# Kernel optimization log

Hardware: AMD Instinct MI355X
Metric: run time of the kernel (lower is better)

## Reference

```python
import jax, jax.numpy as jnp
import numpy as np

N_HEAD = 16
EPS = 1e-6


def setup_inputs() -> dict:
    key = jax.random.key(0)
    k1, k2, k3 = jax.random.split(key, 3)
    B, T, C = 2, 2048, 1024
    x = jax.random.normal(k1, (B, T, C), dtype=jnp.float32)
    w_attn = jax.random.normal(k2, (C, 3 * C), dtype=jnp.float32) * 0.02
    w_proj = jax.random.normal(k3, (C, C), dtype=jnp.float32) * 0.02
    return {"x": x, "w_attn": w_attn, "w_proj": w_proj}


def _linear_attention(q, k, v):
    """q,k,v: (T,B,H,D) with q,k already feature-mapped (elu+1).
    Causal linear attention via a D x D running-state recurrence (same math
    as cumsum of k-v outer products, computed without the O(T*D^2) tensor)."""
    B, H, D = q.shape[1], q.shape[2], q.shape[3]

    def step(carry, qkv_t):
        S, z = carry                      # S:(B,H,D,D), z:(B,H,D)
        qt, kt, vt = qkv_t                # each (B,H,D)
        S = S + kt[..., :, None] * vt[..., None, :]
        z = z + kt
        num = jnp.einsum('bhi,bhij->bhj', qt, S)
        den = jnp.sum(qt * z, axis=-1, keepdims=True)
        return (S, z), num / (den + EPS)

    S0 = jnp.zeros((B, H, D, D), q.dtype)
    z0 = jnp.zeros((B, H, D), q.dtype)
    _, y = jax.lax.scan(step, (S0, z0), (q, k, v))
    return y                              # (T,B,H,D)


def reference(x, w_attn, w_proj):
    B, T, C = x.shape
    H = N_HEAD
    D = C // H
    qkv = x @ w_attn                      # (B,T,3C)
    q, k, v = jnp.split(qkv, 3, axis=-1)

    def to_tbhd(a):                       # (B,T,C) -> (T,B,H,D)
        return a.reshape(B, T, H, D).transpose(1, 0, 2, 3)

    q = jax.nn.elu(to_tbhd(q)) + 1.0      # phi(x) = ELU(x)+1
    k = jax.nn.elu(to_tbhd(k)) + 1.0
    v = to_tbhd(v)

    y = _linear_attention(q, k, v)        # (T,B,H,D)
    y = y.transpose(1, 0, 2, 3).reshape(B, T, C)
    return y @ w_proj                     # resid dropout p=0.0 is identity
```

## Files before the change

kernel.cpp:

```cpp
#include <hip/hip_runtime.h>
#include <hip/hip_bf16.h>
#include <cmath>

#define TB   2048
#define CCH  1024
#define NCH  32
#define EPSF 1e-6f

typedef unsigned short u16;
typedef __attribute__((ext_vector_type(8))) short  frag8;
typedef __attribute__((ext_vector_type(4))) float  floatx4;

__device__ __forceinline__ u16 f2bf(float f) {
    unsigned int u = __float_as_uint(f);
    unsigned int r = (u + 0x7fffu + ((u >> 16) & 1u)) >> 16;
    return (u16)r;
}
__device__ __forceinline__ float bf2f(u16 v) {
    return __uint_as_float(((unsigned int)v) << 16);
}

__device__ __forceinline__ void async_load16(const u16* g, u16* l) {
    __builtin_amdgcn_global_load_lds(
        (const __attribute__((address_space(1))) void*)g,
        (__attribute__((address_space(3))) void*)l,
        16, 0, 0);
}

__global__ __launch_bounds__(256) void prep_k(
    const float* __restrict__ x, const float* __restrict__ wa,
    const float* __restrict__ wp,
    u16* __restrict__ xb, u16* __restrict__ waT, u16* __restrict__ wpT)
{
    __shared__ u16 t[64][72];
    int blk = blockIdx.x;
    if (blk < 2048) {
        int i = (blk * 256 + threadIdx.x) * 8;
        float4 a = *(const float4*)(x + i);
        float4 b = *(const float4*)(x + i + 4);
        u16 v[8];
        v[0] = f2bf(a.x); v[1] = f2bf(a.y); v[2] = f2bf(a.z); v[3] = f2bf(a.w);
        v[4] = f2bf(b.x); v[5] = f2bf(b.y); v[6] = f2bf(b.z); v[7] = f2bf(b.w);
        *(uint4*)(xb + i) = *(uint4*)v;
        return;
    }
    const float* in; u16* out; int K, N, bx, by;
    if (blk < 2048 + 768) {
        int tb = blk - 2048; in = wa; out = waT; K = 1024; N = 3072;
        bx = tb % 48; by = tb / 48;
    } else {
        int tb = blk - 2816; in = wp; out = wpT; K = 1024; N = 1024;
        bx = tb & 15; by = tb >> 4;
    }
    const int k0 = by * 64, n0 = bx * 64;
    #pragma unroll
    for (int i = 0; i < 4; ++i) {
        int rr = (threadIdx.x >> 4) + 16 * i;
        int c4 = (threadIdx.x & 15) * 4;
        float4 v = *(const float4*)(in + (size_t)(k0 + rr) * N + n0 + c4);
        t[c4 + 0][rr] = f2bf(v.x);
        t[c4 + 1][rr] = f2bf(v.y);
        t[c4 + 2][rr] = f2bf(v.z);
        t[c4 + 3][rr] = f2bf(v.w);
    }
    __syncthreads();
    #pragma unroll
    for (int i = 0; i < 2; ++i) {
        int rr = (threadIdx.x >> 3) + 32 * i;
        int c8 = (threadIdx.x & 7) * 8;
        u16 o[8];
        #pragma unroll
        for (int q = 0; q < 8; ++q) o[q] = t[rr][c8 + q];
        *(uint4*)(out + (size_t)(n0 + rr) * K + k0 + c8) = *(uint4*)o;
    }
}

__global__ __launch_bounds__(256) void gemm_bf16_bf16out_k(
    const u16* __restrict__ A, const u16* __restrict__ BT,
    u16* __restrict__ C, int N, int K, int phi_cols)
{
    __shared__ u16 Als[2][128 * 64];
    __shared__ u16 Bls[2][128 * 64];
    const int tid  = threadIdx.x;
    const int wave = tid >> 6, lane = tid & 63;
    const int quad = lane >> 4, lrow = lane & 15;
    const int wm = wave >> 1, wn = wave & 1;
    const int row0 = blockIdx.y * 128, col0 = blockIdx.x * 128;
    const int lr = lane >> 3;
    const int lc = ((lane & 7) ^ lr) * 8;
    const int rsw = lrow & 7;
    floatx4 acc[4][4] = {};
    const int NT = K >> 6;

    #pragma unroll
    for (int m = 0; m < 4; ++m) {
        int i = wave * 4 + m;
        async_load16(A  + (size_t)(row0 + i * 8 + lr) * K + lc, &Als[0][i * 512]);
        async_load16(BT + (size_t)(col0 + i * 8 + lr) * K + lc, &Bls[0][i * 512]);
    }

    for (int t = 0; t < NT; ++t) {
        const int p = t & 1;
        if (t + 1 < NT) {
            const int k0 = (t + 1) << 6;
            #pragma unroll
            for (int m = 0; m < 4; ++m) {
                int i = wave * 4 + m;
                async_load16(A  + (size_t)(row0 + i * 8 + lr) * K + k0 + lc,
                             &Als[p ^ 1][i * 512]);
                async_load16(BT + (size_t)(col0 + i * 8 + lr) * K + k0 + lc,
                             &Bls[p ^ 1][i * 512]);
            }
            __builtin_amdgcn_sched_barrier(0);
            asm volatile("s_waitcnt vmcnt(8)" ::: "memory");
        } else {
            asm volatile("s_waitcnt vmcnt(0)" ::: "memory");
        }
        __builtin_amdgcn_s_barrier();
        __builtin_amdgcn_sched_barrier(0);

        #pragma unroll
        for (int ksi = 0; ksi < 2; ++ksi) {
            frag8 af[4], bf[4];
            #pragma unroll
            for (int i = 0; i < 4; ++i)
                af[i] = *(const frag8*)&Als[p][(wm * 64 + i * 16 + lrow) * 64
                                              + ((ksi * 4 + quad) ^ rsw) * 8];
            #pragma unroll
            for (int i = 0; i < 4; ++i)
                bf[i] = *(const frag8*)&Bls[p][(wn * 64 + i * 16 + lrow) * 64
                                              + ((ksi * 4 + quad) ^ rsw) * 8];
            #pragma unroll
            for (int i = 0; i < 4; ++i)
                #pragma unroll
                for (int jn = 0; jn < 4; ++jn)
                    acc[i][jn] = __builtin_amdgcn_mfma_f32_16x16x32_bf16(
                        af[i], bf[jn], acc[i][jn], 0, 0, 0);
        }

        asm volatile("s_waitcnt lgkmcnt(0)" ::: "memory");
        __builtin_amdgcn_sched_barrier(0);
        __builtin_amdgcn_s_barrier();
    }

    #pragma unroll
    for (int i = 0; i < 4; ++i) {
        #pragma unroll
        for (int jn = 0; jn < 4; ++jn) {
            int col = col0 + wn * 64 + jn * 16 + lrow;
            bool isphi = col < phi_cols;
            #pragma unroll
            for (int r = 0; r < 4; ++r) {
                int row = row0 + wm * 64 + i * 16 + quad * 4 + r;
                float v = acc[i][jn][r];
                if (isphi) v = (v > 0.f) ? (v + 1.f) : __expf(v);
                C[(size_t)row * N + col] = f2bf(v);
            }
        }
    }
}

__global__ __launch_bounds__(256) void gemm_bf16_f32out_k(
    const u16* __restrict__ A, const u16* __restrict__ BT,
    float* __restrict__ C, int N, int K)
{
    __shared__ u16 Als[128 * 128];
    __shared__ u16 Bls[64 * 128];
    const int tid  = threadIdx.x;
    const int wave = tid >> 6, lane = tid & 63;
    const int quad = lane >> 4, lrow = lane & 15;
    const int wm = wave >> 1, wn = wave & 1;
    const int row0 = blockIdx.y * 128, col0 = blockIdx.x * 64;
    const int lr4 = lane >> 4;
    floatx4 acc[4][2] = {};

    for (int k0 = 0; k0 < K; k0 += 128) {
        __syncthreads();
        #pragma unroll
        for (int m = 0; m < 8; ++m) {
            int rbase = wave * 32 + m * 4;
            int cg = (lane & 15) ^ ((rbase + lr4) & 15);
            async_load16(A + (size_t)(row0 + rbase + lr4) * K + k0 + cg * 8,
                         &Als[rbase * 128]);
        }
        #pragma unroll
        for (int m = 0; m < 4; ++m) {
            int rbase = wave * 16 + m * 4;
            int cg = (lane & 15) ^ ((rbase + lr4) & 15);
            async_load16(BT + (size_t)(col0 + rbase + lr4) * K + k0 + cg * 8,
                         &Bls[rbase * 128]);
        }
        __syncthreads();
        #pragma unroll
        for (int ksi = 0; ksi < 4; ++ksi) {
            frag8 af[4], bf[2];
            #pragma unroll
            for (int i = 0; i < 4; ++i)
                af[i] = *(const frag8*)&Als[(wm * 64 + i * 16 + lrow) * 128
                                            + ((ksi * 4 + quad) ^ lrow) * 8];
            #pragma unroll
            for (int jn = 0; jn < 2; ++jn)
                bf[jn] = *(const frag8*)&Bls[(wn * 32 + jn * 16 + lrow) * 128
                                             + ((ksi * 4 + quad) ^ lrow) * 8];
            #pragma unroll
            for (int i = 0; i < 4; ++i)
                #pragma unroll
                for (int jn = 0; jn < 2; ++jn)
                    acc[i][jn] = __builtin_amdgcn_mfma_f32_16x16x32_bf16(
                        af[i], bf[jn], acc[i][jn], 0, 0, 0);
        }
    }

    #pragma unroll
    for (int i = 0; i < 4; ++i)
        #pragma unroll
        for (int jn = 0; jn < 2; ++jn) {
            int col = col0 + wn * 32 + jn * 16 + lrow;
            #pragma unroll
            for (int r = 0; r < 4; ++r) {
                int row = row0 + wm * 64 + i * 16 + quad * 4 + r;
                C[(size_t)row * N + col] = acc[i][jn][r];
            }
        }
}

__global__ __launch_bounds__(256) void chunk_kv_mfma_k(
    const u16* __restrict__ qkv,
    u16* __restrict__ Spt,
    float* __restrict__ zloc,
    u16* __restrict__ VtG)
{
    __shared__ u16 Kt[64][72];
    __shared__ u16 Vt[64][72];
    const int tid  = threadIdx.x;
    const int wave = tid >> 6, lane = tid & 63;
    const int quad = lane >> 4, lrow = lane & 15;
    const int blk = blockIdx.x;
    const int c = blk & 31, h = (blk >> 5) & 15, b = blk >> 9;
    const int t0 = c * 64;
    const u16* base = qkv + (size_t)(b * TB + t0) * 3072 + h * 64;

    #pragma unroll
    for (int m = 0; m < 2; ++m) {
        int chunk = tid + 256 * m;
        int s = chunk >> 3, d0 = (chunk & 7) * 8;
        const u16* row = base + (size_t)s * 3072;
        u16 kv[8], vv[8];
        *(uint4*)kv = *(const uint4*)(row + 1024 + d0);
        *(uint4*)vv = *(const uint4*)(row + 2048 + d0);
        #pragma unroll
        for (int q = 0; q < 8; ++q) { Kt[d0 + q][s] = kv[q]; Vt[d0 + q][s] = vv[q]; }
    }
    __syncthreads();

    #pragma unroll
    for (int m = 0; m < 2; ++m) {
        int e = tid + 256 * m;
        int r = e >> 3, c8 = (e & 7) * 8;
        u16 o[8];
        #pragma unroll
        for (int q = 0; q < 8; ++q) o[q] = Vt[r][c8 + q];
        *(uint4*)(VtG + (size_t)blk * 4096 + r * 64 + c8) = *(uint4*)o;
    }

    frag8 vf[2];
    #pragma unroll
    for (int ks = 0; ks < 2; ++ks)
        vf[ks] = *(const frag8*)&Vt[wave * 16 + lrow][ks * 32 + quad * 8];
    u16* So = Spt + (size_t)blk * 4096;
    #pragma unroll
    for (int jn = 0; jn < 4; ++jn) {
        floatx4 acc = {};
        #pragma unroll
        for (int ks = 0; ks < 2; ++ks) {
            frag8 kf = *(const frag8*)&Kt[jn * 16 + lrow][ks * 32 + quad * 8];
            acc = __builtin_amdgcn_mfma_f32_16x16x32_bf16(vf[ks], kf, acc, 0, 0, 0);
        }
        #pragma unroll
        for (int r = 0; r < 4; ++r) {
            int j = wave * 16 + quad * 4 + r;
            int i = jn * 16 + lrow;
            So[j * 64 + i] = f2bf(acc[r]);
        }
    }
    if (tid < 64) {
        float z = 0.f;
        for (int s = 0; s < 64; ++s) z += bf2f(Kt[tid][s]);
        zloc[(size_t)blk * 64 + tid] = z;
    }
}

__global__ __launch_bounds__(256) void scan_state_k(
    u16* __restrict__ Spt, float* __restrict__ z)
{
    const int bh = blockIdx.x >> 1;
    const int part = blockIdx.x & 1;
    const int e0 = part * 2048 + threadIdx.x * 8;
    const size_t base = (size_t)bh * NCH * 4096;
    float r[8] = {};
    for (int c = 0; c < NCH; ++c) {
        u16* p = Spt + base + (size_t)c * 4096 + e0;
        u16 t[8];
        *(uint4*)t = *(const uint4*)p;
        u16 o[8];
        #pragma unroll
        for (int q = 0; q < 8; ++q) { o[q] = f2bf(r[q]); r[q] += bf2f(t[q]); }
        *(uint4*)p = *(uint4*)o;
    }
    if (part == 0 && threadIdx.x < 64) {
        const size_t zb = (size_t)bh * NCH * 64;
        float rz = 0.f;
        for (int c = 0; c < NCH; ++c) {
            float t = z[zb + c * 64 + threadIdx.x];
            z[zb + c * 64 + threadIdx.x] = rz;
            rz += t;
        }
    }
}

__global__ __launch_bounds__(256) void attn_mfma_k(
    const u16* __restrict__ qkv,
    const u16* __restrict__ SptG,
    const float* __restrict__ zp,
    const u16* __restrict__ VtG,
    u16* __restrict__ Yb)
{
    __shared__ u16 Qls[64 * 64];
    __shared__ u16 Kls[64 * 64];
    __shared__ u16 Vls[64 * 64];
    __shared__ u16 Sls[64 * 64];
    __shared__ float zps[64];
    __shared__ float den4[64][4];
    __shared__ float den[64];

    const int tid  = threadIdx.x;
    const int wave = tid >> 6, lane = tid & 63;
    const int quad = lane >> 4, lrow = lane & 15;
    const int blk = blockIdx.x;
    const int c = blk & 31, h = (blk >> 5) & 15, b = blk >> 9;
    const int t0 = c * 64;
    const int lr = lane >> 3;
    const int lc = ((lane & 7) ^ lr) * 8;
    const int rsw = lrow & 7;
    const u16* qbase = qkv + (size_t)(b * TB + t0) * 3072 + h * 64;

    #pragma unroll
    for (int m = 0; m < 2; ++m) {
        int i = wave * 2 + m;
        int r = i * 8 + lr;
        async_load16(qbase + (size_t)r * 3072 + lc,          &Qls[i * 512]);
        async_load16(qbase + (size_t)r * 3072 + 1024 + lc,   &Kls[i * 512]);
        async_load16(SptG + (size_t)blk * 4096 + r * 64 + lc, &Sls[i * 512]);
        async_load16(VtG  + (size_t)blk * 4096 + r * 64 + lc, &Vls[i * 512]);
    }
    if (tid < 64) zps[tid] = zp[(size_t)blk * 64 + tid];
    __syncthreads();

    frag8 qf[2];
    #pragma unroll
    for (int ks = 0; ks < 2; ++ks)
        qf[ks] = *(const frag8*)&Qls[(wave * 16 + lrow) * 64 + ((ks * 4 + quad) ^ rsw) * 8];

    floatx4 yacc[4] = {}, kacc[4] = {};
    #pragma unroll
    for (int jn = 0; jn < 4; ++jn) {
        #pragma unroll
        for (int ks = 0; ks < 2; ++ks) {
            frag8 spf = *(const frag8*)&Sls[(jn * 16 + lrow) * 64 + ((ks * 4 + quad) ^ rsw) * 8];
            yacc[jn] = __builtin_amdgcn_mfma_f32_16x16x32_bf16(qf[ks], spf, yacc[jn], 0, 0, 0);
            frag8 kf = *(const frag8*)&Kls[(jn * 16 + lrow) * 64 + ((ks * 4 + quad) ^ rsw) * 8];
            kacc[jn] = __builtin_amdgcn_mfma_f32_16x16x32_bf16(qf[ks], kf, kacc[jn], 0, 0, 0);
        }
    }
    __syncthreads();

    #pragma unroll
    for (int jn = 0; jn < 4; ++jn) {
        int s = jn * 16 + lrow;
        #pragma unroll
        for (int r = 0; r < 4; ++r) {
            int t = wave * 16 + quad * 4 + r;
            float v = (s <= t) ? kacc[jn][r] : 0.f;
            Sls[t * 64 + (((s >> 3) ^ (t & 7)) * 8) + (s & 7)] = f2bf(v);
        }
    }
    __syncthreads();

    {
        int t = tid >> 2, seg = tid & 3;
        float p = 0.f;
        #pragma unroll
        for (int g2 = 0; g2 < 2; ++g2) {
            int g = seg * 2 + g2;
            int pq = ((g ^ (t & 7)) * 8);
            const u16* qp = &Qls[t * 64 + pq];
            const u16* ap = &Sls[t * 64 + pq];
            #pragma unroll
            for (int e = 0; e < 8; ++e) {
                p += bf2f(qp[e]) * zps[g * 8 + e] + bf2f(ap[e]);
            }
        }
        den4[t][seg] = p;
    }

    frag8 af2[2];
    #pragma unroll
    for (int ks = 0; ks < 2; ++ks)
        af2[ks] = *(const frag8*)&Sls[(wave * 16 + lrow) * 64 + ((ks * 4 + quad) ^ rsw) * 8];
    #pragma unroll
    for (int jn = 0; jn < 4; ++jn)
        #pragma unroll
        for (int ks = 0; ks < 2; ++ks) {
            frag8 vf = *(const frag8*)&Vls[(jn * 16 + lrow) * 64 + ((ks * 4 + quad) ^ rsw) * 8];
            yacc[jn] = __builtin_amdgcn_mfma_f32_16x16x32_bf16(af2[ks], vf, yacc[jn], 0, 0, 0);
        }
    __syncthreads();
    if (tid < 64) den[tid] = den4[tid][0] + den4[tid][1] + den4[tid][2] + den4[tid][3];
    __syncthreads();

    #pragma unroll
    for (int jn = 0; jn < 4; ++jn) {
        #pragma unroll
        for (int r = 0; r < 4; ++r) {
            int t = wave * 16 + quad * 4 + r;
            float inv = 1.f / (den[t] + EPSF);
            Qls[t * 64 + jn * 16 + lrow] = f2bf(yacc[jn][r] * inv);
        }
    }
    __syncthreads();
    {
        int row = tid >> 2, seg = tid & 3;
        size_t o = (size_t)(b * TB + t0 + row) * CCH + h * 64 + seg * 16;
        *(uint4*)(Yb + o)     = *(uint4*)&Qls[row * 64 + seg * 16];
        *(uint4*)(Yb + o + 8) = *(uint4*)&Qls[row * 64 + seg * 16 + 8];
    }
}

extern "C" void kernel_launch(void* const* d_in, const int* in_sizes, int n_in,
                              void* d_out, int out_size, void* d_ws, size_t ws_size,
                              hipStream_t stream)
{
    const float* x      = (const float*)d_in[0];
    const float* w_attn = (const float*)d_in[1];
    const float* w_proj = (const float*)d_in[2];
    float* out = (float*)d_out;

    u16* xb    = (u16*)d_ws;
    u16* waT   = xb    + (size_t)4096 * 1024;
    u16* wpT   = waT   + (size_t)3072 * 1024;
    u16* Yb    = wpT   + (size_t)1024 * 1024;
    u16* qkv_b = Yb    + (size_t)4096 * 1024;
    u16* Spt   = qkv_b + (size_t)4096 * 3072;
    u16* VtG   = Spt   + (size_t)1024 * 4096;
    float* zloc = (float*)(VtG + (size_t)1024 * 4096);

    prep_k<<<3072, 256, 0, stream>>>(x, w_attn, w_proj, xb, waT, wpT);

    gemm_bf16_bf16out_k<<<dim3(24, 32), 256, 0, stream>>>(xb, waT, qkv_b, 3072, 1024, 2048);

    chunk_kv_mfma_k<<<1024, 256, 0, stream>>>(qkv_b, Spt, zloc, VtG);
    scan_state_k   <<<64,   256, 0, stream>>>(Spt, zloc);
    attn_mfma_k    <<<1024, 256, 0, stream>>>(qkv_b, Spt, zloc, VtG, Yb);

    gemm_bf16_f32out_k<<<dim3(16, 32), 256, 0, stream>>>(Yb, wpT, out, 1024, 1024);
}
```

Baseline: 166.8 us.

## Widen QKV GEMM tiles, double-buffer output GEMM, split state scan wider

The QKV projection GEMM now uses 128x192 tiles (6 B-fragments per wave), so it launches 512 blocks instead of 768. That count fits more evenly across the CUs and raises reuse of each A tile. The output projection GEMM switches from single-buffered K=128 stages with two syncthreads to a double-buffered K=64 async-load pipeline, which overlaps global loads with MFMA work. The state scan is split across twice as many blocks with 4 elements per thread to expose more parallelism. The risks are higher register pressure from the 24 accumulators with a 2-block occupancy hint, and a larger LDS footprint.

```diff
diff --git a/kernel.cpp b/kernel.cpp
--- a/kernel.cpp
+++ b/kernel.cpp
@@ -75,27 +75,31 @@
     }
 }
 
-__global__ __launch_bounds__(256) void gemm_bf16_bf16out_k(
+__global__ __launch_bounds__(256, 2) void gemm1_k(
     const u16* __restrict__ A, const u16* __restrict__ BT,
     u16* __restrict__ C, int N, int K, int phi_cols)
 {
     __shared__ u16 Als[2][128 * 64];
-    __shared__ u16 Bls[2][128 * 64];
+    __shared__ u16 Bls[2][192 * 64];
     const int tid  = threadIdx.x;
     const int wave = tid >> 6, lane = tid & 63;
     const int quad = lane >> 4, lrow = lane & 15;
     const int wm = wave >> 1, wn = wave & 1;
-    const int row0 = blockIdx.y * 128, col0 = blockIdx.x * 128;
+    const int row0 = blockIdx.y * 128, col0 = blockIdx.x * 192;
     const int lr = lane >> 3;
     const int lc = ((lane & 7) ^ lr) * 8;
     const int rsw = lrow & 7;
-    floatx4 acc[4][4] = {};
+    floatx4 acc[4][6] = {};
     const int NT = K >> 6;
 
     #pragma unroll
     for (int m = 0; m < 4; ++m) {
         int i = wave * 4 + m;
-        async_load16(A  + (size_t)(row0 + i * 8 + lr) * K + lc, &Als[0][i * 512]);
+        async_load16(A + (size_t)(row0 + i * 8 + lr) * K + lc, &Als[0][i * 512]);
+    }
+    #pragma unroll
+    for (int m = 0; m < 6; ++m) {
+        int i = wave * 6 + m;
         async_load16(BT + (size_t)(col0 + i * 8 + lr) * K + lc, &Bls[0][i * 512]);
     }
 
@@ -106,13 +110,17 @@
             #pragma unroll
             for (int m = 0; m < 4; ++m) {
                 int i = wave * 4 + m;
-                async_load16(A  + (size_t)(row0 + i * 8 + lr) * K + k0 + lc,
+                async_load16(A + (size_t)(row0 + i * 8 + lr) * K + k0 + lc,
                              &Als[p ^ 1][i * 512]);
+            }
+            #pragma unroll
+            for (int m = 0; m < 6; ++m) {
+                int i = wave * 6 + m;
                 async_load16(BT + (size_t)(col0 + i * 8 + lr) * K + k0 + lc,
                              &Bls[p ^ 1][i * 512]);
             }
             __builtin_amdgcn_sched_barrier(0);
-            asm volatile("s_waitcnt vmcnt(8)" ::: "memory");
+            asm volatile("s_waitcnt vmcnt(10)" ::: "memory");
         } else {
             asm volatile("s_waitcnt vmcnt(0)" ::: "memory");
         }
@@ -121,21 +129,21 @@
 
         #pragma unroll
         for (int ksi = 0; ksi < 2; ++ksi) {
-            frag8 af[4], bf[4];
+            frag8 af[4], bf[6];
             #pragma unroll
             for (int i = 0; i < 4; ++i)
                 af[i] = *(const frag8*)&Als[p][(wm * 64 + i * 16 + lrow) * 64
                                               + ((ksi * 4 + quad) ^ rsw) * 8];
             #pragma unroll
-            for (int i = 0; i < 4; ++i)
-                bf[i] = *(const frag8*)&Bls[p][(wn * 64 + i * 16 + lrow) * 64
+            for (int j = 0; j < 6; ++j)
+                bf[j] = *(const frag8*)&Bls[p][(wn * 96 + j * 16 + lrow) * 64
                                               + ((ksi * 4 + quad) ^ rsw) * 8];
             #pragma unroll
             for (int i = 0; i < 4; ++i)
                 #pragma unroll
-                for (int jn = 0; jn < 4; ++jn)
-                    acc[i][jn] = __builtin_amdgcn_mfma_f32_16x16x32_bf16(
-                        af[i], bf[jn], acc[i][jn], 0, 0, 0);
+                for (int j = 0; j < 6; ++j)
+                    acc[i][j] = __builtin_amdgcn_mfma_f32_16x16x32_bf16(
+                        af[i], bf[j], acc[i][j], 0, 0, 0);
         }
 
         asm volatile("s_waitcnt lgkmcnt(0)" ::: "memory");
@@ -146,13 +154,13 @@
     #pragma unroll
     for (int i = 0; i < 4; ++i) {
         #pragma unroll
-        for (int jn = 0; jn < 4; ++jn) {
-            int col = col0 + wn * 64 + jn * 16 + lrow;
+        for (int j = 0; j < 6; ++j) {
+            int col = col0 + wn * 96 + j * 16 + lrow;
             bool isphi = col < phi_cols;
             #pragma unroll
             for (int r = 0; r < 4; ++r) {
                 int row = row0 + wm * 64 + i * 16 + quad * 4 + r;
-                float v = acc[i][jn][r];
+                float v = acc[i][j][r];
                 if (isphi) v = (v > 0.f) ? (v + 1.f) : __expf(v);
                 C[(size_t)row * N + col] = f2bf(v);
             }
@@ -160,48 +168,69 @@
     }
 }
 
-__global__ __launch_bounds__(256) void gemm_bf16_f32out_k(
+__global__ __launch_bounds__(256, 2) void gemm_bf16_f32out_k(
     const u16* __restrict__ A, const u16* __restrict__ BT,
     float* __restrict__ C, int N, int K)
 {
-    __shared__ u16 Als[128 * 128];
-    __shared__ u16 Bls[64 * 128];
+    __shared__ u16 Als[2][128 * 64];
+    __shared__ u16 Bls[2][64 * 64];
     const int tid  = threadIdx.x;
     const int wave = tid >> 6, lane = tid & 63;
     const int quad = lane >> 4, lrow = lane & 15;
     const int wm = wave >> 1, wn = wave & 1;
     const int row0 = blockIdx.y * 128, col0 = blockIdx.x * 64;
-    const int lr4 = lane >> 4;
+    const int lr = lane >> 3;
+    const int lc = ((lane & 7) ^ lr) * 8;
+    const int rsw = lrow & 7;
     floatx4 acc[4][2] = {};
-
-    for (int k0 = 0; k0 < K; k0 += 128) {
-        __syncthreads();
-        #pragma unroll
-        for (int m = 0; m < 8; ++m) {
-            int rbase = wave * 32 + m * 4;
-            int cg = (lane & 15) ^ ((rbase + lr4) & 15);
-            async_load16(A + (size_t)(row0 + rbase + lr4) * K + k0 + cg * 8,
-                         &Als[rbase * 128]);
-        }
-        #pragma unroll
-        for (int m = 0; m < 4; ++m) {
-            int rbase = wave * 16 + m * 4;
-            int cg = (lane & 15) ^ ((rbase + lr4) & 15);
-            async_load16(BT + (size_t)(col0 + rbase + lr4) * K + k0 + cg * 8,
-                         &Bls[rbase * 128]);
-        }
-        __syncthreads();
-        #pragma unroll
-        for (int ksi = 0; ksi < 4; ++ksi) {
+    const int NT = K >> 6;
+
+    #pragma unroll
+    for (int m = 0; m < 4; ++m) {
+        int i = wave * 4 + m;
+        async_load16(A + (size_t)(row0 + i * 8 + lr) * K + lc, &Als[0][i * 512]);
+    }
+    #pragma unroll
+    for (int m = 0; m < 2; ++m) {
+        int i = wave * 2 + m;
+        async_load16(BT + (size_t)(col0 + i * 8 + lr) * K + lc, &Bls[0][i * 512]);
+    }
+
+    for (int t = 0; t < NT; ++t) {
+        const int p = t & 1;
+        if (t + 1 < NT) {
+            const int k0 = (t + 1) << 6;
+            #pragma unroll
+            for (int m = 0; m < 4; ++m) {
+                int i = wave * 4 + m;
+                async_load16(A + (size_t)(row0 + i * 8 + lr) * K + k0 + lc,
+                             &Als[p ^ 1][i * 512]);
+            }
+            #pragma unroll
+            for (int m = 0; m < 2; ++m) {
+                int i = wave * 2 + m;
+                async_load16(BT + (size_t)(col0 + i * 8 + lr) * K + k0 + lc,
+                             &Bls[p ^ 1][i * 512]);
+            }
+            __builtin_amdgcn_sched_barrier(0);
+            asm volatile("s_waitcnt vmcnt(6)" ::: "memory");
+        } else {
+            asm volatile("s_waitcnt vmcnt(0)" ::: "memory");
+        }
+        __builtin_amdgcn_s_barrier();
+        __builtin_amdgcn_sched_barrier(0);
+
+        #pragma unroll
+        for (int ksi = 0; ksi < 2; ++ksi) {
             frag8 af[4], bf[2];
             #pragma unroll
             for (int i = 0; i < 4; ++i)
-                af[i] = *(const frag8*)&Als[(wm * 64 + i * 16 + lrow) * 128
-                                            + ((ksi * 4 + quad) ^ lrow) * 8];
+                af[i] = *(const frag8*)&Als[p][(wm * 64 + i * 16 + lrow) * 64
+                                              + ((ksi * 4 + quad) ^ rsw) * 8];
             #pragma unroll
             for (int jn = 0; jn < 2; ++jn)
-                bf[jn] = *(const frag8*)&Bls[(wn * 32 + jn * 16 + lrow) * 128
-                                             + ((ksi * 4 + quad) ^ lrow) * 8];
+                bf[jn] = *(const frag8*)&Bls[p][(wn * 32 + jn * 16 + lrow) * 64
+                                               + ((ksi * 4 + quad) ^ rsw) * 8];
             #pragma unroll
             for (int i = 0; i < 4; ++i)
                 #pragma unroll
@@ -209,6 +238,10 @@
                     acc[i][jn] = __builtin_amdgcn_mfma_f32_16x16x32_bf16(
                         af[i], bf[jn], acc[i][jn], 0, 0, 0);
         }
+
+        asm volatile("s_waitcnt lgkmcnt(0)" ::: "memory");
+        __builtin_amdgcn_sched_barrier(0);
+        __builtin_amdgcn_s_barrier();
     }
 
     #pragma unroll
@@ -293,19 +326,19 @@
 __global__ __launch_bounds__(256) void scan_state_k(
     u16* __restrict__ Spt, float* __restrict__ z)
 {
-    const int bh = blockIdx.x >> 1;
-    const int part = blockIdx.x & 1;
-    const int e0 = part * 2048 + threadIdx.x * 8;
+    const int bh = blockIdx.x >> 2;
+    const int part = blockIdx.x & 3;
+    const int e0 = part * 1024 + threadIdx.x * 4;
     const size_t base = (size_t)bh * NCH * 4096;
-    float r[8] = {};
+    float r[4] = {};
     for (int c = 0; c < NCH; ++c) {
         u16* p = Spt + base + (size_t)c * 4096 + e0;
-        u16 t[8];
-        *(uint4*)t = *(const uint4*)p;
-        u16 o[8];
-        #pragma unroll
-        for (int q = 0; q < 8; ++q) { o[q] = f2bf(r[q]); r[q] += bf2f(t[q]); }
-        *(uint4*)p = *(uint4*)o;
+        u16 t[4];
+        *(uint2*)t = *(const uint2*)p;
+        u16 o[4];
+        #pragma unroll
+        for (int q = 0; q < 4; ++q) { o[q] = f2bf(r[q]); r[q] += bf2f(t[q]); }
+        *(uint2*)p = *(uint2*)o;
     }
     if (part == 0 && threadIdx.x < 64) {
         const size_t zb = (size_t)bh * NCH * 64;
@@ -456,10 +489,10 @@
 
     prep_k<<<3072, 256, 0, stream>>>(x, w_attn, w_proj, xb, waT, wpT);
 
-    gemm_bf16_bf16out_k<<<dim3(24, 32), 256, 0, stream>>>(xb, waT, qkv_b, 3072, 1024, 2048);
+    gemm1_k<<<dim3(16, 32), 256, 0, stream>>>(xb, waT, qkv_b, 3072, 1024, 2048);
 
     chunk_kv_mfma_k<<<1024, 256, 0, stream>>>(qkv_b, Spt, zloc, VtG);
-    scan_state_k   <<<64,   256, 0, stream>>>(Spt, zloc);
+    scan_state_k   <<<128,  256, 0, stream>>>(Spt, zloc);
     attn_mfma_k    <<<1024, 256, 0, stream>>>(qkv_b, Spt, zloc, VtG, Yb);
 
     gemm_bf16_f32out_k<<<dim3(16, 32), 256, 0, stream>>>(Yb, wpT, out, 1024, 1024);
```

Result: faster. 154.7 us, median of 2 (-7.2%).
